# Performance work log

Hardware: AMD Instinct MI355X
Metric: run time of the kernel (lower is better)

The kernel has to match this reference:

```python
import jax, jax.numpy as jnp
import numpy as np

M = 1024       # input feature dim
T_EXPERTS = 64 # number of experts
K = 2          # top-k
TOKENS = 65536 # B*N flattened tokens


def setup_inputs() -> dict:
    key = jax.random.key(0)
    ks = jax.random.split(key, 6)
    return {
        "x": jax.random.normal(ks[0], (TOKENS, M), dtype=jnp.float32),
        "noise": jax.random.normal(ks[1], (TOKENS, T_EXPERTS), dtype=jnp.float32),
        "Wg_w": jax.random.normal(ks[2], (T_EXPERTS, M), dtype=jnp.float32) * 0.02,
        "Wg_b": jax.random.normal(ks[3], (T_EXPERTS,), dtype=jnp.float32) * 0.02,
        "Wn_w": jax.random.normal(ks[4], (T_EXPERTS, M), dtype=jnp.float32) * 0.02,
        "Wn_b": jax.random.normal(ks[5], (T_EXPERTS,), dtype=jnp.float32) * 0.02,
    }


def reference(x, noise, Wg_w, Wg_b, Wn_w, Wn_b):
    # logits = Wg(x); noise_scale = softplus(Wnoise(x))
    logits = jnp.einsum("bm,tm->bt", x, Wg_w) + Wg_b          # [tokens, t]
    noise_scale = jax.nn.softplus(jnp.einsum("bm,tm->bt", x, Wn_w) + Wn_b)
    H = logits + noise * noise_scale                           # noisy logits
    topk_vals, topk_idx = jax.lax.top_k(H, K)                  # [tokens, k]
    topk_softmax = jax.nn.softmax(topk_vals, axis=-1)
    # scatter softmax weights into sparse [tokens, t] gate tensor
    rows = jnp.arange(H.shape[0])[:, None]
    gates = jnp.zeros_like(H).at[rows, topk_idx].set(topk_softmax)
    return (gates, H, topk_idx, noise_scale, logits)
```

## Files before the change

kernel.cpp:

```cpp
#include <hip/hip_runtime.h>
#include <math.h>

#define NTOK 65536
#define MDIM 1024
#define NE   64
#define TB   128
#define NKC  32
#define DELTA 5e-4f

typedef float f32x4  __attribute__((ext_vector_type(4)));
typedef short bf16x8 __attribute__((ext_vector_type(8)));
typedef unsigned int u32;

__device__ __forceinline__ unsigned short f32_to_bf16_rne(float f) {
    u32 u = __builtin_bit_cast(u32, f);
    u32 r = u + 0x7FFFu + ((u >> 16) & 1u);
    return (unsigned short)(r >> 16);
}
__device__ __forceinline__ float bf16_to_f32(unsigned short h) {
    u32 u = ((u32)h) << 16;
    return __builtin_bit_cast(float, u);
}
__device__ __forceinline__ void gll16(const void* g, void* l) {
    __builtin_amdgcn_global_load_lds(
        (const __attribute__((address_space(1))) u32*)g,
        (__attribute__((address_space(3))) u32*)l, 16, 0, 0);
}

__global__ __launch_bounds__(256) void split_w_kernel(
    const float* __restrict__ Wg_w, const float* __restrict__ Wn_w,
    unsigned short* __restrict__ ws, u32* __restrict__ cnt)
{
    if (blockIdx.x == 0 && threadIdx.x == 0) *cnt = 0;

    const int gid  = blockIdx.x * 256 + threadIdx.x;
    const int kc   = gid >> 10;
    const int rest = gid & 1023;
    const int tm   = rest >> 8;
    const int mat  = (rest >> 7) & 1;
    const int sp   = (rest >> 6) & 1;
    const int lane = rest & 63;
    const int e    = (lane & 15) + 16 * tm;
    const int k0   = kc * 32 + 8 * (lane >> 4);
    const float* W = mat ? Wn_w : Wg_w;

    unsigned short o[8];
#pragma unroll
    for (int i = 0; i < 8; ++i) {
        const float v = W[(size_t)e * MDIM + k0 + i];
        const u32 u  = __builtin_bit_cast(u32, v);
        const unsigned short hb = (unsigned short)(u >> 16);
        o[i] = sp ? f32_to_bf16_rne(v - bf16_to_f32(hb)) : hb;
    }
    uint4 pk;
    pk.x = (u32)o[0] | ((u32)o[1] << 16);
    pk.y = (u32)o[2] | ((u32)o[3] << 16);
    pk.z = (u32)o[4] | ((u32)o[5] << 16);
    pk.w = (u32)o[6] | ((u32)o[7] << 16);
    *reinterpret_cast<uint4*>(&ws[(size_t)gid * 8]) = pk;
}

__global__ __launch_bounds__(512, 4) void gate_mfma_kernel(
    const float* __restrict__ x,
    const float* __restrict__ noise,
    const unsigned short* __restrict__ ws,
    const float* __restrict__ Wg_b,
    const float* __restrict__ Wn_b,
    float* __restrict__ out_gates,
    float* __restrict__ out_H,
    float* __restrict__ out_idx,
    float* __restrict__ out_ns,
    float* __restrict__ out_logits,
    u32* __restrict__ cnt,
    u32* __restrict__ list)
{
    __shared__ unsigned short wbuf[2][8192];

    const int tid   = threadIdx.x;
    const int lane  = tid & 63;
    const int w     = tid >> 6;
    const int c     = lane & 15;
    const int q     = lane >> 4;
    const int tokw  = blockIdx.x * TB + w * 16;
    const int phase = blockIdx.x & 31;

    const float* __restrict__ xr = x + (size_t)(tokw + c) * MDIM + 8 * q;

    f32x4 acc[4][2];
#pragma unroll
    for (int tm = 0; tm < 4; ++tm)
#pragma unroll
        for (int m = 0; m < 2; ++m)
            acc[tm][m] = (f32x4){0.f, 0.f, 0.f, 0.f};

    {
        const unsigned short* w0 = ws + (size_t)phase * 8192;
        gll16(w0 + (size_t)tid * 8,         &wbuf[0][(size_t)tid * 8]);
        gll16(w0 + (size_t)(tid + 512) * 8, &wbuf[0][(size_t)(tid + 512) * 8]);
    }
    __builtin_amdgcn_sched_barrier(0);
    f32x4 xa = *reinterpret_cast<const f32x4*>(xr + phase * 32);
    f32x4 xb = *reinterpret_cast<const f32x4*>(xr + phase * 32 + 4);
    __builtin_amdgcn_sched_barrier(0);
    asm volatile("s_waitcnt vmcnt(2)" ::: "memory");
    __syncthreads();

    int cur = 0;
    for (int kci = 0; kci < NKC; ++kci) {
        asm volatile("s_waitcnt vmcnt(0)" ::: "memory");

        bf16x8 xhi, xlo;
        {
            const float v[8] = {xa.x, xa.y, xa.z, xa.w, xb.x, xb.y, xb.z, xb.w};
            u32 hp[4], lp[4];
#pragma unroll
            for (int p = 0; p < 4; ++p) {
                const u32 u0 = __builtin_bit_cast(u32, v[2 * p]);
                const u32 u1 = __builtin_bit_cast(u32, v[2 * p + 1]);
                const float h0 = __builtin_bit_cast(float, u0 & 0xFFFF0000u);
                const float h1 = __builtin_bit_cast(float, u1 & 0xFFFF0000u);
                hp[p] = (u0 >> 16) | (u1 & 0xFFFF0000u);
                const u32 l0 = (u32)f32_to_bf16_rne(v[2 * p] - h0);
                const u32 l1 = (u32)f32_to_bf16_rne(v[2 * p + 1] - h1);
                lp[p] = l0 | (l1 << 16);
            }
            const uint4 h4 = {hp[0], hp[1], hp[2], hp[3]};
            const uint4 l4 = {lp[0], lp[1], lp[2], lp[3]};
            xhi = __builtin_bit_cast(bf16x8, h4);
            xlo = __builtin_bit_cast(bf16x8, l4);
        }

        if (kci + 1 < NKC) {
            const int kcn = (kci + 1 + phase) & 31;
            const unsigned short* wc = ws + (size_t)kcn * 8192;
            gll16(wc + (size_t)tid * 8,         &wbuf[cur ^ 1][(size_t)tid * 8]);
            gll16(wc + (size_t)(tid + 512) * 8, &wbuf[cur ^ 1][(size_t)(tid + 512) * 8]);
            __builtin_amdgcn_sched_barrier(0);
            const int off = kcn * 32;
            xa = *reinterpret_cast<const f32x4*>(xr + off);
            xb = *reinterpret_cast<const f32x4*>(xr + off + 4);
            __builtin_amdgcn_sched_barrier(0);
        }

#pragma unroll
        for (int tm = 0; tm < 4; ++tm)
#pragma unroll
            for (int mat = 0; mat < 2; ++mat) {
                const int gbase = ((tm * 4 + mat * 2) * 64 + lane) * 8;
                const bf16x8 whi = *reinterpret_cast<const bf16x8*>(&wbuf[cur][gbase]);
                const bf16x8 wlo = *reinterpret_cast<const bf16x8*>(&wbuf[cur][gbase + 512]);
                f32x4 a = acc[tm][mat];
                a = __builtin_amdgcn_mfma_f32_16x16x32_bf16(wlo, xhi, a, 0, 0, 0);
                a = __builtin_amdgcn_mfma_f32_16x16x32_bf16(whi, xlo, a, 0, 0, 0);
                a = __builtin_amdgcn_mfma_f32_16x16x32_bf16(whi, xhi, a, 0, 0, 0);
                acc[tm][mat] = a;
            }

        if (kci + 1 < NKC) {
            asm volatile("s_waitcnt vmcnt(2)" ::: "memory");
            __syncthreads();
        }
        cur ^= 1;
    }

    f32x4 bgv[4], bnv[4];
#pragma unroll
    for (int tm = 0; tm < 4; ++tm) {
        bgv[tm] = *reinterpret_cast<const f32x4*>(&Wg_b[16 * tm + 4 * q]);
        bnv[tm] = *reinterpret_cast<const f32x4*>(&Wn_b[16 * tm + 4 * q]);
    }

    const int tok = tokw + c;
    float hv[4][4];

#pragma unroll
    for (int tm = 0; tm < 4; ++tm) {
        const size_t rb = (size_t)tok * NE + 16 * tm + 4 * q;
        const f32x4 nz = *reinterpret_cast<const f32x4*>(&noise[rb]);
        f32x4 lg, nsv, hh;
#pragma unroll
        for (int r = 0; r < 4; ++r) {
            lg[r] = acc[tm][0][r] + bgv[tm][r];
            const float nl = acc[tm][1][r] + bnv[tm][r];
            nsv[r] = fmaxf(nl, 0.f) + log1pf(expf(-fabsf(nl)));
            hh[r]  = fmaf(nz[r], nsv[r], lg[r]);
            hv[tm][r] = hh[r];
        }
        *reinterpret_cast<f32x4*>(&out_logits[rb]) = lg;
        *reinterpret_cast<f32x4*>(&out_ns[rb])     = nsv;
        *reinterpret_cast<f32x4*>(&out_H[rb])      = hh;
    }

    float v1 = -INFINITY, v2 = -INFINITY, v3 = -INFINITY;
    int   i1 = 0,         i2 = 0;
#pragma unroll
    for (int tm = 0; tm < 4; ++tm)
#pragma unroll
        for (int r = 0; r < 4; ++r) {
            const int ex = 16 * tm + 4 * q + r;
            const float hcur = hv[tm][r];
            if (hcur > v1)      { v3 = v2; v2 = v1; i2 = i1; v1 = hcur; i1 = ex; }
            else if (hcur > v2) { v3 = v2; v2 = hcur; i2 = ex; }
            else if (hcur > v3) { v3 = hcur; }
        }

#pragma unroll
    for (int off = 16; off <= 32; off <<= 1) {
        const float w1 = __shfl_xor(v1, off, 64);
        const int   k1 = __shfl_xor(i1, off, 64);
        const float w2 = __shfl_xor(v2, off, 64);
        const int   k2 = __shfl_xor(i2, off, 64);
        const float w3 = __shfl_xor(v3, off, 64);
        float m3;
        if (v1 >= w1) m3 = (v2 >= w1) ? fmaxf(v3, w1) : fmaxf(v2, w2);
        else          m3 = (w2 >= v1) ? fmaxf(w3, v1) : fmaxf(w2, v2);
        if (w1 > v1 || (w1 == v1 && k1 < i1)) {
            if (v1 > w2 || (v1 == w2 && i1 < k2)) { v2 = v1; i2 = i1; }
            else                                  { v2 = w2; i2 = k2; }
            v1 = w1; i1 = k1;
        } else {
            if (w1 > v2 || (w1 == v2 && k1 < i2)) { v2 = w1; i2 = k1; }
        }
        v3 = m3;
    }

    const float e2v = expf(v2 - v1);
    const float inv = 1.f / (1.f + e2v);
    const float p1  = inv;
    const float p2  = e2v * inv;

#pragma unroll
    for (int tm = 0; tm < 4; ++tm) {
        f32x4 g;
#pragma unroll
        for (int r = 0; r < 4; ++r) {
            const int ex = 16 * tm + 4 * q + r;
            g[r] = (ex == i1) ? p1 : ((ex == i2) ? p2 : 0.f);
        }
        *reinterpret_cast<f32x4*>(&out_gates[(size_t)tok * NE + 16 * tm + 4 * q]) = g;
    }
    if (q == 0) {
        *reinterpret_cast<float2*>(&out_idx[(size_t)tok * 2]) =
            make_float2((float)i1, (float)i2);
        if ((v1 - v2 < DELTA) || (v2 - v3 < DELTA)) {
            const u32 slot = atomicAdd(cnt, 1u);
            list[slot] = (u32)tok;
        }
    }
}

__global__ __launch_bounds__(64) void refine_kernel(
    const float* __restrict__ x,
    const float* __restrict__ noise,
    const float* __restrict__ Wg_w, const float* __restrict__ Wg_b,
    const float* __restrict__ Wn_w, const float* __restrict__ Wn_b,
    const u32* __restrict__ cnt, const u32* __restrict__ list,
    float* __restrict__ out_gates, float* __restrict__ out_idx)
{
    const int lane = threadIdx.x;
    const u32 n = *cnt;

    for (u32 it = blockIdx.x; it < n; it += gridDim.x) {
        const int tok = (int)list[it];

        f32x4 xv[4];
#pragma unroll
        for (int i = 0; i < 4; ++i)
            xv[i] = *reinterpret_cast<const f32x4*>(
                &x[(size_t)tok * MDIM + lane * 16 + i * 4]);

        float lgv = 0.f, nlv = 0.f;
        for (int e = 0; e < NE; ++e) {
            float sg = 0.f, sn = 0.f;
#pragma unroll
            for (int i = 0; i < 4; ++i) {
                const f32x4 wg = *reinterpret_cast<const f32x4*>(
                    &Wg_w[(size_t)e * MDIM + lane * 16 + i * 4]);
                const f32x4 wn = *reinterpret_cast<const f32x4*>(
                    &Wn_w[(size_t)e * MDIM + lane * 16 + i * 4]);
#pragma unroll
                for (int j = 0; j < 4; ++j) {
                    sg = fmaf(xv[i][j], wg[j], sg);
                    sn = fmaf(xv[i][j], wn[j], sn);
                }
            }
#pragma unroll
            for (int off = 32; off >= 1; off >>= 1) {
                sg += __shfl_xor(sg, off, 64);
                sn += __shfl_xor(sn, off, 64);
            }
            if (e == lane) { lgv = sg; nlv = sn; }
        }

        lgv += Wg_b[lane];
        nlv += Wn_b[lane];
        const float ns = fmaxf(nlv, 0.f) + log1pf(expf(-fabsf(nlv)));
        const float h  = fmaf(noise[(size_t)tok * NE + lane], ns, lgv);

        float v1 = h; int i1 = lane;
#pragma unroll
        for (int off = 32; off >= 1; off >>= 1) {
            const float ov = __shfl_xor(v1, off, 64);
            const int   oi = __shfl_xor(i1, off, 64);
            if (ov > v1 || (ov == v1 && oi < i1)) { v1 = ov; i1 = oi; }
        }
        float v2 = (lane == i1) ? -INFINITY : h; int i2 = lane;
#pragma unroll
        for (int off = 32; off >= 1; off >>= 1) {
            const float ov = __shfl_xor(v2, off, 64);
            const int   oi = __shfl_xor(i2, off, 64);
            if (ov > v2 || (ov == v2 && oi < i2)) { v2 = ov; i2 = oi; }
        }

        const float e2v = expf(v2 - v1);
        const float inv = 1.f / (1.f + e2v);
        const float p1  = inv;
        const float p2  = e2v * inv;

        out_gates[(size_t)tok * NE + lane] =
            (lane == i1) ? p1 : ((lane == i2) ? p2 : 0.f);
        if (lane == 0) {
            *reinterpret_cast<float2*>(&out_idx[(size_t)tok * 2]) =
                make_float2((float)i1, (float)i2);
        }
    }
}

extern "C" void kernel_launch(void* const* d_in, const int* in_sizes, int n_in,
                              void* d_out, int out_size, void* d_ws, size_t ws_size,
                              hipStream_t stream) {
    const float* x     = (const float*)d_in[0];
    const float* noise = (const float*)d_in[1];
    const float* Wg_w  = (const float*)d_in[2];
    const float* Wg_b  = (const float*)d_in[3];
    const float* Wn_w  = (const float*)d_in[4];
    const float* Wn_b  = (const float*)d_in[5];

    float* out = (float*)d_out;
    float* out_gates  = out;
    float* out_H      = out + (size_t)NTOK * NE;
    float* out_idx    = out + (size_t)2 * NTOK * NE;
    float* out_ns     = out + (size_t)2 * NTOK * NE + (size_t)NTOK * 2;
    float* out_logits = out + (size_t)3 * NTOK * NE + (size_t)NTOK * 2;

    unsigned short* wsplit = (unsigned short*)d_ws;
    u32* cnt  = (u32*)((char*)d_ws + 524288);
    u32* list = (u32*)((char*)d_ws + 524304);

    split_w_kernel<<<dim3(128), dim3(256), 0, stream>>>(Wg_w, Wn_w, wsplit, cnt);
    gate_mfma_kernel<<<dim3(NTOK / TB), dim3(512), 0, stream>>>(
        x, noise, wsplit, Wg_b, Wn_b,
        out_gates, out_H, out_idx, out_ns, out_logits, cnt, list);
    refine_kernel<<<dim3(1024), dim3(64), 0, stream>>>(
        x, noise, Wg_w, Wg_b, Wn_w, Wn_b, cnt, list, out_gates, out_idx);
}
```

Measured before the change: 137.5 us.

## Triple-buffer weight LDS stages and prefetch two K-chunks ahead

Replaces the double-buffered LDS weight pipeline with a triple buffer and double-buffered x registers, so each iteration issues loads two chunks ahead. It waits with vmcnt(4) and uses a single barrier per iteration instead of a full drain plus a second barrier. The loop is fully unrolled. This is meant to hide global/LDS load latency behind the MFMA work. In exchange it uses 50% more LDS, which may reduce occupancy, and adds register pressure.

```diff
diff --git a/kernel.cpp b/kernel.cpp
--- a/kernel.cpp
+++ b/kernel.cpp
@@ -74,7 +74,7 @@
     u32* __restrict__ cnt,
     u32* __restrict__ list)
 {
-    __shared__ unsigned short wbuf[2][8192];
+    __shared__ unsigned short wbuf[3][8192];
 
     const int tid   = threadIdx.x;
     const int lane  = tid & 63;
@@ -82,7 +82,7 @@
     const int c     = lane & 15;
     const int q     = lane >> 4;
     const int tokw  = blockIdx.x * TB + w * 16;
-    const int phase = blockIdx.x & 31;
+    const int phase = blockIdx.x & (NKC - 1);
 
     const float* __restrict__ xr = x + (size_t)(tokw + c) * MDIM + 8 * q;
 
@@ -93,25 +93,43 @@
         for (int m = 0; m < 2; ++m)
             acc[tm][m] = (f32x4){0.f, 0.f, 0.f, 0.f};
 
-    {
-        const unsigned short* w0 = ws + (size_t)phase * 8192;
-        gll16(w0 + (size_t)tid * 8,         &wbuf[0][(size_t)tid * 8]);
-        gll16(w0 + (size_t)(tid + 512) * 8, &wbuf[0][(size_t)(tid + 512) * 8]);
-    }
-    __builtin_amdgcn_sched_barrier(0);
-    f32x4 xa = *reinterpret_cast<const f32x4*>(xr + phase * 32);
-    f32x4 xb = *reinterpret_cast<const f32x4*>(xr + phase * 32 + 4);
-    __builtin_amdgcn_sched_barrier(0);
-    asm volatile("s_waitcnt vmcnt(2)" ::: "memory");
-    __syncthreads();
-
-    int cur = 0;
-    for (int kci = 0; kci < NKC; ++kci) {
-        asm volatile("s_waitcnt vmcnt(0)" ::: "memory");
+    f32x4 xa[2], xb[2];
+
+#define STAGE(I, BUF, SET)                                                      \
+    {                                                                           \
+        const int ci_ = ((I) + phase) & (NKC - 1);                              \
+        const unsigned short* wc_ = ws + (size_t)ci_ * 8192;                    \
+        gll16(wc_ + (size_t)tid * 8,         &wbuf[BUF][(size_t)tid * 8]);      \
+        gll16(wc_ + (size_t)(tid + 512) * 8, &wbuf[BUF][(size_t)(tid + 512) * 8]); \
+        __builtin_amdgcn_sched_barrier(0);                                      \
+        xa[SET] = *reinterpret_cast<const f32x4*>(xr + ci_ * 32);               \
+        xb[SET] = *reinterpret_cast<const f32x4*>(xr + ci_ * 32 + 4);           \
+        __builtin_amdgcn_sched_barrier(0);                                      \
+    }
+
+    STAGE(0, 0, 0)
+    STAGE(1, 1, 1)
+
+#pragma unroll
+    for (int i = 0; i < NKC; ++i) {
+        const int set = i & 1;
+        const int bcur = i % 3;
+        const int bstg = (i + 2) % 3;
+
+        if (i < NKC - 1) {
+            asm volatile("s_waitcnt vmcnt(4)" ::: "memory");
+        } else {
+            asm volatile("s_waitcnt vmcnt(0)" ::: "memory");
+        }
+        __builtin_amdgcn_sched_barrier(0);
+        __builtin_amdgcn_s_barrier();
+        __builtin_amdgcn_sched_barrier(0);
 
         bf16x8 xhi, xlo;
         {
-            const float v[8] = {xa.x, xa.y, xa.z, xa.w, xb.x, xb.y, xb.z, xb.w};
+            const f32x4 a = xa[set];
+            const f32x4 b = xb[set];
+            const float v[8] = {a.x, a.y, a.z, a.w, b.x, b.y, b.z, b.w};
             u32 hp[4], lp[4];
 #pragma unroll
             for (int p = 0; p < 4; ++p) {
@@ -129,17 +147,10 @@
             xhi = __builtin_bit_cast(bf16x8, h4);
             xlo = __builtin_bit_cast(bf16x8, l4);
         }
-
-        if (kci + 1 < NKC) {
-            const int kcn = (kci + 1 + phase) & 31;
-            const unsigned short* wc = ws + (size_t)kcn * 8192;
-            gll16(wc + (size_t)tid * 8,         &wbuf[cur ^ 1][(size_t)tid * 8]);
-            gll16(wc + (size_t)(tid + 512) * 8, &wbuf[cur ^ 1][(size_t)(tid + 512) * 8]);
-            __builtin_amdgcn_sched_barrier(0);
-            const int off = kcn * 32;
-            xa = *reinterpret_cast<const f32x4*>(xr + off);
-            xb = *reinterpret_cast<const f32x4*>(xr + off + 4);
-            __builtin_amdgcn_sched_barrier(0);
+        __builtin_amdgcn_sched_barrier(0);
+
+        if (i + 2 < NKC) {
+            STAGE(i + 2, bstg, set)
         }
 
 #pragma unroll
@@ -147,21 +158,16 @@
 #pragma unroll
             for (int mat = 0; mat < 2; ++mat) {
                 const int gbase = ((tm * 4 + mat * 2) * 64 + lane) * 8;
-                const bf16x8 whi = *reinterpret_cast<const bf16x8*>(&wbuf[cur][gbase]);
-                const bf16x8 wlo = *reinterpret_cast<const bf16x8*>(&wbuf[cur][gbase + 512]);
+                const bf16x8 whi = *reinterpret_cast<const bf16x8*>(&wbuf[bcur][gbase]);
+                const bf16x8 wlo = *reinterpret_cast<const bf16x8*>(&wbuf[bcur][gbase + 512]);
                 f32x4 a = acc[tm][mat];
                 a = __builtin_amdgcn_mfma_f32_16x16x32_bf16(wlo, xhi, a, 0, 0, 0);
                 a = __builtin_amdgcn_mfma_f32_16x16x32_bf16(whi, xlo, a, 0, 0, 0);
                 a = __builtin_amdgcn_mfma_f32_16x16x32_bf16(whi, xhi, a, 0, 0, 0);
                 acc[tm][mat] = a;
             }
-
-        if (kci + 1 < NKC) {
-            asm volatile("s_waitcnt vmcnt(2)" ::: "memory");
-            __syncthreads();
-        }
-        cur ^= 1;
-    }
+    }
+#undef STAGE
 
     f32x4 bgv[4], bnv[4];
 #pragma unroll
```

New measurement: 139.8 us. About the same (+1.7%).
